# Kernel tuning notes

Measured on AMD Instinct MI355X. Metric: run time of the kernel, lower is better.

## Reference

```python
import jax, jax.numpy as jnp
import numpy as np

NF, IN_NF, N_LAYERS = 64, 196, 3
B, H, W = 1, 256, 256
P3 = [(1, 1), (1, 1)]
P1 = [(0, 0), (0, 0)]


def conv2d(x, w, pad):
    return jax.lax.conv_general_dilated(x, w, (1, 1), pad,
                                        dimension_numbers=('NCHW', 'OIHW', 'NCHW'))


def prelu(x, a):
    return jnp.where(x >= 0, x, a[None, :, None, None] * x)


def warp(x, flow):
    # standard backward bilinear warp, zero padding outside the image
    Bx, C, Hx, Wx = x.shape
    yy, xx = jnp.meshgrid(jnp.arange(Hx, dtype=x.dtype),
                          jnp.arange(Wx, dtype=x.dtype), indexing='ij')
    px = xx[None] + flow[:, 0]  # (B,H,W)
    py = yy[None] + flow[:, 1]

    def sample(img, px, py):  # img (C,H,W); px,py (H,W)
        x0 = jnp.floor(px)
        y0 = jnp.floor(py)
        x1 = x0 + 1.0
        y1 = y0 + 1.0
        wx1 = px - x0
        wx0 = 1.0 - wx1
        wy1 = py - y0
        wy0 = 1.0 - wy1

        def gather(xi, yi):
            valid = (xi >= 0) & (xi <= Wx - 1) & (yi >= 0) & (yi <= Hx - 1)
            xc = jnp.clip(xi, 0, Wx - 1).astype(jnp.int32)
            yc = jnp.clip(yi, 0, Hx - 1).astype(jnp.int32)
            return img[:, yc, xc] * valid.astype(img.dtype)

        return (gather(x0, y0) * (wx0 * wy0) + gather(x1, y0) * (wx1 * wy0)
                + gather(x0, y1) * (wx0 * wy1) + gather(x1, y1) * (wx1 * wy1))

    return jax.vmap(sample)(x, px, py)


def setup_inputs() -> dict:
    key = jax.random.key(0)
    ks = jax.random.split(key, 11)
    s = 0.05
    return {
        'feat_0': jax.random.normal(ks[0], (B, 64, H, W), jnp.float32),
        'feat_1': jax.random.normal(ks[1], (B, 64, H, W), jnp.float32),
        'feat_dense': jax.random.normal(ks[2], (B, 64, H, W), jnp.float32),
        'flow': jax.random.normal(ks[3], (B, 4, H, W), jnp.float32),
        'space_mask': jax.random.uniform(ks[4], (B, 1, H, W), jnp.float32),
        'head_w': jax.random.normal(ks[5], (IN_NF, IN_NF, 3, 3), jnp.float32) * s,
        'head_a': jnp.full((IN_NF,), 0.25, jnp.float32),
        'conv_w': jax.random.normal(ks[6], (N_LAYERS, IN_NF, IN_NF, 3, 3), jnp.float32) * s,
        'conv_a': jnp.full((N_LAYERS, IN_NF), 0.25, jnp.float32),
        'last_w': jax.random.normal(ks[7], (4 + NF, IN_NF * (N_LAYERS + 1), 1, 1), jnp.float32) * s,
        'last_b': jax.random.normal(ks[8], (4 + NF,), jnp.float32) * s,
        'mask_w': jax.random.normal(ks[9], (2, NF, 3, 3), jnp.float32) * s,
        'mask_b': jax.random.normal(ks[10], (2,), jnp.float32) * s,
    }


def reference(feat_0, feat_1, feat_dense, flow, space_mask,
              head_w, head_a, conv_w, conv_a, last_w, last_b, mask_w, mask_b):
    f0 = warp(feat_0, flow[:, :2])
    f1 = warp(feat_1, flow[:, 2:4])
    x = jnp.concatenate([f0, f1, feat_dense, flow], axis=1)  # (B, in_nf, H, W)
    sm_up = jnp.repeat(jnp.repeat(space_mask, 2, axis=2), 2, axis=3)

    # head: conv3x3 -> PReLU, then mask (dense / use_sparsity=False path)
    x = prelu(conv2d(x, head_w, P3), head_a) * space_mask
    outs = [x]
    for i in range(N_LAYERS):
        x = conv2d(x, conv_w[i], P3) * space_mask
        x = prelu(x, conv_a[i])
        outs.append(x)
    x = conv2d(jnp.concatenate(outs, axis=1), last_w, P1) + last_b[None, :, None, None]

    smn = conv2d(x[:, 4:], mask_w, P3) + mask_b[None, :, None, None]

    Bx, Cx, Hx, Wx = x.shape
    x_up = jax.image.resize(x, (Bx, Cx, 2 * Hx, 2 * Wx), method='bilinear')
    smn_up = jax.image.resize(smn, (Bx, 2, 2 * Hx, 2 * Wx), method='bilinear')

    flow_out = x_up[:, :4]
    feat_t = x_up[:, 4:]
    # eval-mode mask (training=False): hard argmax between channel 0 and 1
    mask_next = (smn_up[:, :1] > smn_up[:, 1:2]).astype(x.dtype) * sm_up
    return flow_out, feat_t, mask_next
```

## Files before the change

### kernel.cpp

```cpp
#include <hip/hip_runtime.h>

typedef _Float16 f16;
typedef _Float16 f16x8 __attribute__((ext_vector_type(8)));
typedef _Float16 f16x4 __attribute__((ext_vector_type(4)));
typedef float    f32x4 __attribute__((ext_vector_type(4)));
typedef float    f32x16 __attribute__((ext_vector_type(16)));

#define MFMA16(a,b,c) __builtin_amdgcn_mfma_f32_16x16x32_f16(a,b,c,0,0,0)
#define MFMA32(a,b,c) __builtin_amdgcn_mfma_f32_32x32x16_f16(a,b,c,0,0,0)

#define NPIX 65536
#define PXS   8
#define KHS   2064
#define K16S  4128
#define HS    8256
#define CBS   16512
#define ROWH  115584
#define RBYTES 231168
#define SBUF  ((size_t)258*RBYTES)

#define PKSUB  7168
#define PKCB   43008
#define PK_CONV 903168

#define PKL_CB  5120
#define PKL_BI  35840

#define ASTG 14336
#define BSTG 16640

__global__ void k_pack_conv(const float* __restrict__ head_w,
                            const float* __restrict__ conv_w,
                            f16* __restrict__ dst)
{
    int t = blockIdx.x*256 + threadIdx.x;
    int lane = t & 63; t >>= 6;
    int ob  = t % 7;  t /= 7;
    int sel = t & 1;  t >>= 1;
    int kx  = t % 3;  t /= 3;
    int k16 = t & 1;  t >>= 1;
    int cb  = t % 7;  t /= 7;
    int ky  = t % 3;  t /= 3;
    int li  = t;
    if (li >= 4) return;
    const float* W = (li == 0) ? head_w : (conv_w + (size_t)(li-1)*196*196*9);
    int oc  = ob*32 + (lane & 31);
    int ic0 = cb*32 + k16*16 + (lane >> 5)*8;
    int tap = ky*3 + kx;
    f16x8 v;
#pragma unroll
    for (int j = 0; j < 8; ++j) {
        int ic = ic0 + j;
        float x = 0.f;
        if (oc < 196 && ic < 196) x = W[((size_t)oc*196 + ic)*9 + tap];
        f16 h = (f16)x;
        v[j] = (sel == 0) ? h : (f16)(x - (float)h);
    }
    size_t frag = (((((size_t)(ky*7+cb)*2 + k16)*3 + kx)*2 + sel)*7 + ob);
    *(f16x8*)(dst + (size_t)li*PK_CONV + frag*512 + (size_t)lane*8) = v;
}

__global__ void k_pack_last(const float* __restrict__ last_w, f16* __restrict__ dst)
{
    int t = blockIdx.x*256 + threadIdx.x;
    if (t >= 4*7*5*2*64) return;
    int lane = t & 63; t >>= 6;
    int sel  = t & 1;  t >>= 1;
    int ob   = t % 5;  t /= 5;
    int cb   = t % 7;  t /= 7;
    int bi   = t;
    int oc = ob*16 + (lane & 15);
    int k0 = cb*32 + (lane >> 4)*8;
    f16x8 v;
#pragma unroll
    for (int j = 0; j < 8; ++j) {
        int k = k0 + j;
        float x = 0.f;
        if (oc < 68 && k < 196) x = last_w[(size_t)oc*784 + bi*196 + k];
        f16 h = (f16)x;
        v[j] = (sel == 0) ? h : (f16)(x - (float)h);
    }
    *(f16x8*)(dst + (((size_t)((bi*7+cb)*5 + ob)*2 + sel)*64 + lane)*8) = v;
}

__global__ void k_zero_halo(f16* __restrict__ bufA, f16* __restrict__ bufB)
{
    int c = blockIdx.x*256 + threadIdx.x;
    int end = c & 1; c >>= 1;
    int kh  = c & 1; c >>= 1;
    int k16 = c & 1; c >>= 1;
    int h   = c & 1; c >>= 1;
    int cb  = c % 7; c /= 7;
    int row = c % 258; c /= 258;
    if (c >= 2) return;
    f16* base = (c == 0) ? bufA : bufB;
    f16* p = base + (size_t)row*ROWH + cb*CBS + h*HS + k16*K16S + kh*KHS + (end ? 257 : 0)*PXS;
    f16x8 z = {(f16)0,(f16)0,(f16)0,(f16)0,(f16)0,(f16)0,(f16)0,(f16)0};
    *(f16x8*)p = z;
}

struct Gath { int o00,o01,o10,o11; float w00,w01,w10,w11; };

__device__ inline Gath mk_gath(float pxf, float pyf)
{
    float x0 = floorf(pxf), y0 = floorf(pyf);
    float x1 = x0 + 1.f, y1 = y0 + 1.f;
    float wx1 = pxf - x0, wx0 = 1.f - wx1;
    float wy1 = pyf - y0, wy0 = 1.f - wy1;
    bool vx0 = (x0 >= 0.f) && (x0 <= 255.f);
    bool vx1 = (x1 >= 0.f) && (x1 <= 255.f);
    bool vy0 = (y0 >= 0.f) && (y0 <= 255.f);
    bool vy1 = (y1 >= 0.f) && (y1 <= 255.f);
    int ix0 = min(max((int)x0, 0), 255);
    int ix1 = min(max((int)x1, 0), 255);
    int iy0 = min(max((int)y0, 0), 255);
    int iy1 = min(max((int)y1, 0), 255);
    Gath g;
    g.o00 = iy0*256 + ix0; g.w00 = (vx0 && vy0) ? wx0*wy0 : 0.f;
    g.o01 = iy0*256 + ix1; g.w01 = (vx1 && vy0) ? wx1*wy0 : 0.f;
    g.o10 = iy1*256 + ix0; g.w10 = (vx0 && vy1) ? wx0*wy1 : 0.f;
    g.o11 = iy1*256 + ix1; g.w11 = (vx1 && vy1) ? wx1*wy1 : 0.f;
    return g;
}

__device__ inline void store4n(f16* __restrict__ rowb, int slot, int c0,
                               float a, float b, float c, float d)
{
    f16x4 hi, lo;
    f16 h;
    h = (f16)a; hi[0] = h; lo[0] = (f16)(a - (float)h);
    h = (f16)b; hi[1] = h; lo[1] = (f16)(b - (float)h);
    h = (f16)c; hi[2] = h; lo[2] = (f16)(c - (float)h);
    h = (f16)d; hi[3] = h; lo[3] = (f16)(d - (float)h);
    int cb = c0 >> 5, w32 = c0 & 31;
    f16* p = rowb + cb*CBS + (w32 >> 4)*K16S + ((w32 >> 3) & 1)*KHS
                 + (size_t)slot*PXS + (w32 & 7);
    *(f16x4*)p        = hi;
    *(f16x4*)(p + HS) = lo;
}

__global__ void k_warp_concat(const float* __restrict__ f0, const float* __restrict__ f1,
                              const float* __restrict__ fd, const float* __restrict__ flow,
                              f16* __restrict__ out)
{
    int px = blockIdx.x*256 + threadIdx.x;
    int row = px >> 8, col = px & 255;
    f16* rowb = out + (size_t)(row+1)*ROWH;
    int slot = col + 1;
    Gath g0 = mk_gath((float)col + flow[px],          (float)row + flow[NPIX   + px]);
    Gath g1 = mk_gath((float)col + flow[2*NPIX + px], (float)row + flow[3*NPIX + px]);
#pragma unroll
    for (int c = 0; c < 64; c += 4) {
        float v[4];
#pragma unroll
        for (int r = 0; r < 4; ++r) {
            const float* im = f0 + (size_t)(c+r)*NPIX;
            v[r] = g0.w00*im[g0.o00] + g0.w01*im[g0.o01] + g0.w10*im[g0.o10] + g0.w11*im[g0.o11];
        }
        store4n(rowb, slot, c, v[0], v[1], v[2], v[3]);
    }
#pragma unroll
    for (int c = 0; c < 64; c += 4) {
        float v[4];
#pragma unroll
        for (int r = 0; r < 4; ++r) {
            const float* im = f1 + (size_t)(c+r)*NPIX;
            v[r] = g1.w00*im[g1.o00] + g1.w01*im[g1.o01] + g1.w10*im[g1.o10] + g1.w11*im[g1.o11];
        }
        store4n(rowb, slot, 64 + c, v[0], v[1], v[2], v[3]);
    }
#pragma unroll
    for (int c = 0; c < 64; c += 4) {
        store4n(rowb, slot, 128 + c, fd[(size_t)(c+0)*NPIX + px], fd[(size_t)(c+1)*NPIX + px],
                                     fd[(size_t)(c+2)*NPIX + px], fd[(size_t)(c+3)*NPIX + px]);
    }
    store4n(rowb, slot, 192, flow[px], flow[NPIX+px], flow[2*NPIX+px], flow[3*NPIX+px]);
#pragma unroll
    for (int c = 196; c < 224; c += 4) store4n(rowb, slot, c, 0.f, 0.f, 0.f, 0.f);
}

template<int NOB, int OB0>
__device__ __forceinline__ void micro(const char* __restrict__ ab, const char* __restrict__ bl,
                                      f32x16 (&acc)[4][2], int lane)
{
    f16x8 Bh[2], Bl[2];
    Bh[0] = *(const f16x8*)(bl);
    Bh[1] = *(const f16x8*)(bl + 512);
    Bl[0] = *(const f16x8*)(bl + 8320);
    Bl[1] = *(const f16x8*)(bl + 8320 + 512);
#pragma unroll
    for (int o = 0; o < NOB; ++o) {
        f16x8 Ah = *(const f16x8*)(ab + (OB0 + o)*1024 + lane*16);
        f16x8 Al = *(const f16x8*)(ab + (7 + OB0 + o)*1024 + lane*16);
#pragma unroll
        for (int pt = 0; pt < 2; ++pt) {
            acc[o][pt] = MFMA32(Ah, Bh[pt], acc[o][pt]);
            acc[o][pt] = MFMA32(Al, Bh[pt], acc[o][pt]);
            acc[o][pt] = MFMA32(Ah, Bl[pt], acc[o][pt]);
        }
    }
}

__global__ __launch_bounds__(256, 2)
void k_conv32(const f16* __restrict__ in, f16* __restrict__ out,
              const f16* __restrict__ pack, const float* __restrict__ alpha,
              const float* __restrict__ mask)
{
    __shared__ __align__(16) char As[2][ASTG];
    __shared__ __align__(16) char Bs[2][BSTG];

    int bid = blockIdx.x;
    int wg  = (bid & 7)*64 + (bid >> 3);
    int row  = wg >> 1;
    int half = wg & 1;
    int tid  = threadIdx.x;
    int lane = tid & 63;
    int w    = tid >> 6;
    int ocg  = ((w >> 1) ^ bid) & 1;
    int pxg  = w & 1;
    int l31 = lane & 31, lk = lane >> 5;
    int cb0 = half*128;

    f32x16 acc[4][2];
#pragma unroll
    for (int o = 0; o < 4; ++o)
#pragma unroll
        for (int pt = 0; pt < 2; ++pt)
#pragma unroll
            for (int e = 0; e < 16; ++e) acc[o][pt][e] = 0.f;

    auto stageA = [&](int b, const f16* src) {
        __builtin_amdgcn_global_load_lds(
            (const __attribute__((address_space(1))) void*)(src + (size_t)tid*8),
            (__attribute__((address_space(3))) void*)(&As[b][0] + tid*16), 16, 0, 0);
        __builtin_amdgcn_global_load_lds(
            (const __attribute__((address_space(1))) void*)(src + (size_t)(tid+256)*8),
            (__attribute__((address_space(3))) void*)(&As[b][0] + (tid+256)*16), 16, 0, 0);
        __builtin_amdgcn_global_load_lds(
            (const __attribute__((address_space(1))) void*)(src + (size_t)(tid+512)*8),
            (__attribute__((address_space(3))) void*)(&As[b][0] + (tid+512)*16), 16, 0, 0);
        if (tid < 128)
            __builtin_amdgcn_global_load_lds(
                (const __attribute__((address_space(1))) void*)(src + (size_t)(tid+768)*8),
                (__attribute__((address_space(3))) void*)(&As[b][0] + (tid+768)*16), 16, 0, 0);
    };

    auto stageB = [&](int b, const f16* g) {
#pragma unroll
        for (int u = 0; u < 5; ++u) {
            int c = tid + u*256;
            if (u < 4 || c < 1040) {
                int pl = c / 130;
                int i  = c - pl*130;
                const f16* src = g + (size_t)pl*KHS + (size_t)(cb0 + i)*PXS;
                __builtin_amdgcn_global_load_lds(
                    (const __attribute__((address_space(1))) void*)src,
                    (__attribute__((address_space(3))) void*)(&Bs[b][0] + c*16),
                    16, 0, 0);
            }
        }
    };

    const int lbase = lk*2080 + (pxg*64 + l31)*16;

    const f16* g = in + (size_t)row*ROWH;
    stageB(0, g);
    stageA(0, pack);
    __syncthreads();

    int asel = 0, bsel = 0, cbc = 0, q = 0;
    for (int ph = 0; ph < 21; ++ph) {
        if (ph < 20) {
            if (cbc < 6) { g += CBS; ++cbc; }
            else         { g += ROWH - 6*CBS; cbc = 0; }
            stageB(bsel ^ 1, g);
        }
#pragma unroll
        for (int s = 0; s < 6; ++s) {
            if (q < 125) stageA(asel ^ 1, pack + (size_t)(q+1)*PKSUB);
            const char* ab = &As[asel][0];
            const char* bl = &Bs[bsel][0] + lbase + (s/3)*4160 + (s%3)*16;
            if (ocg == 0) micro<4,0>(ab, bl, acc, lane);
            else          micro<3,4>(ab, bl, acc, lane);
            __syncthreads();
            asel ^= 1; ++q;
        }
        bsel ^= 1;
    }

    int nob = (ocg == 0) ? 4 : 3;
    int ob0 = (ocg == 0) ? 0 : 4;
    int colbase = cb0 + pxg*64;
    float mv[2];
#pragma unroll
    for (int pt = 0; pt < 2; ++pt) mv[pt] = mask[row*256 + colbase + pt*32 + l31];
#pragma unroll
    for (int o = 0; o < 4; ++o) {
        if (o >= nob) continue;
        int ob = ob0 + o;
#pragma unroll
        for (int qg = 0; qg < 4; ++qg) {
            int oc0 = ob*32 + 8*qg + 4*lk;
            f32x4 a4 = *(const f32x4*)(alpha + min(oc0, 192));
#pragma unroll
            for (int pt = 0; pt < 2; ++pt) {
                f16x4 hi, lo;
#pragma unroll
                for (int e = 0; e < 4; ++e) {
                    float v = acc[o][pt][qg*4 + e];
                    v = (v >= 0.f ? v : a4[e]*v) * mv[pt];
                    f16 h = (f16)v;
                    hi[e] = h;
                    lo[e] = (f16)(v - (float)h);
                }
                f16* p = out + (size_t)(row+1)*ROWH + (size_t)(colbase + pt*32 + l31 + 1)*PXS
                       + lk*4 + ob*CBS + (qg >> 1)*K16S + (qg & 1)*KHS;
                *(f16x4*)p        = hi;
                *(f16x4*)(p + HS) = lo;
            }
        }
    }
}

__global__ __launch_bounds__(256, 4)
void k_acc_last(const f16* __restrict__ in, const f16* __restrict__ pack,
                const float* __restrict__ bias, float* __restrict__ accp, int bi)
{
    int lane = threadIdx.x & 63;
    int wid  = (blockIdx.x << 2) | (threadIdx.x >> 6);
    int row  = wid >> 3;
    int col0 = (wid & 7) << 5;
    int l15 = lane & 15, lk = lane >> 4;

    f32x4 acc[5][2];
#pragma unroll
    for (int i = 0; i < 5; ++i)
#pragma unroll
        for (int j = 0; j < 2; ++j)
            acc[i][j] = (f32x4){0.f, 0.f, 0.f, 0.f};

    const f16* bb = in + (size_t)(row+1)*ROWH + (size_t)(col0 + l15 + 1)*PXS
                  + (lk >> 1)*K16S + (lk & 1)*KHS;
    const f16* ap = pack + (size_t)bi*PKL_BI + (size_t)lane*8;
    for (int cb = 0; cb < 7; ++cb) {
        f16x8 bh[2], bl[2];
#pragma unroll
        for (int pb = 0; pb < 2; ++pb) {
            const f16* p = bb + cb*CBS + pb*16*PXS;
            bh[pb] = *(const f16x8*)p;
            bl[pb] = *(const f16x8*)(p + HS);
        }
        const f16* a = ap + cb*PKL_CB;
#pragma unroll
        for (int ob = 0; ob < 5; ++ob) {
            f16x8 ah = *(const f16x8*)(a + ob*1024);
            f16x8 al = *(const f16x8*)(a + ob*1024 + 512);
#pragma unroll
            for (int pb = 0; pb < 2; ++pb) {
                acc[ob][pb] = MFMA16(ah, bh[pb], acc[ob][pb]);
                acc[ob][pb] = MFMA16(ah, bl[pb], acc[ob][pb]);
                acc[ob][pb] = MFMA16(al, bh[pb], acc[ob][pb]);
            }
        }
    }
#pragma unroll
    for (int ob = 0; ob < 5; ++ob) {
        int oc0 = ob*16 + lk*4;
        if (oc0 >= 72) continue;
#pragma unroll
        for (int pb = 0; pb < 2; ++pb) {
            int px = row*256 + col0 + pb*16 + l15;
            float* dst = accp + (size_t)px*72 + oc0;
            f32x4 d = acc[ob][pb];
            if (bi == 0) {
                f32x4 b4;
#pragma unroll
                for (int r = 0; r < 4; ++r) b4[r] = bias[min(oc0 + r, 67)];
                *(f32x4*)dst = d + b4;
            } else {
                *(f32x4*)dst = *(const f32x4*)dst + d;
            }
        }
    }
}

__global__ void k_smn(const float* __restrict__ accp, const float* __restrict__ mw,
                      const float* __restrict__ mb, float* __restrict__ smn)
{
    int px = blockIdx.x*256 + threadIdx.x;
    int row = px >> 8, col = px & 255;
    float s0 = mb[0], s1 = mb[1];
    for (int ky = 0; ky < 3; ++ky) {
        int r = row + ky - 1;
        if ((unsigned)r > 255u) continue;
        for (int kx = 0; kx < 3; ++kx) {
            int c = col + kx - 1;
            if ((unsigned)c > 255u) continue;
            const float* ab = accp + ((size_t)r*256 + c)*72 + 4;
            const float* w  = mw + ky*3 + kx;
#pragma unroll
            for (int ch = 0; ch < 64; ch += 4) {
                f32x4 v = *(const f32x4*)(ab + ch);
                s0 += v[0]*w[(ch+0)*9] + v[1]*w[(ch+1)*9] + v[2]*w[(ch+2)*9] + v[3]*w[(ch+3)*9];
                s1 += v[0]*w[(64+ch+0)*9] + v[1]*w[(64+ch+1)*9] + v[2]*w[(64+ch+2)*9] + v[3]*w[(64+ch+3)*9];
            }
        }
    }
    smn[px]        = s0;
    smn[NPIX + px] = s1;
}

__global__ void k_upsample(const float* __restrict__ accp, float* __restrict__ outp)
{
    int o = blockIdx.x*256 + threadIdx.x;
    int oy = o >> 9, ox = o & 511;
    int my = oy >> 1, mx = ox >> 1;
    int r0, r1, c0, c1; float wy0, wy1, wx0, wx1;
    if (oy & 1) { r0 = my;            r1 = min(my+1, 255); wy0 = 0.75f; wy1 = 0.25f; }
    else        { r0 = max(my-1, 0);  r1 = my;             wy0 = 0.25f; wy1 = 0.75f; }
    if (ox & 1) { c0 = mx;            c1 = min(mx+1, 255); wx0 = 0.75f; wx1 = 0.25f; }
    else        { c0 = max(mx-1, 0);  c1 = mx;             wx0 = 0.25f; wx1 = 0.75f; }
    const float* p00 = accp + ((size_t)r0*256 + c0)*72;
    const float* p01 = accp + ((size_t)r0*256 + c1)*72;
    const float* p10 = accp + ((size_t)r1*256 + c0)*72;
    const float* p11 = accp + ((size_t)r1*256 + c1)*72;
    float w00 = wy0*wx0, w01 = wy0*wx1, w10 = wy1*wx0, w11 = wy1*wx1;
#pragma unroll
    for (int ch = 0; ch < 68; ch += 4) {
        f32x4 va = *(const f32x4*)(p00 + ch);
        f32x4 vb = *(const f32x4*)(p01 + ch);
        f32x4 vc = *(const f32x4*)(p10 + ch);
        f32x4 vd = *(const f32x4*)(p11 + ch);
        f32x4 v;
#pragma unroll
        for (int r = 0; r < 4; ++r)
            v[r] = w00*va[r] + w01*vb[r] + w10*vc[r] + w11*vd[r];
        outp[(size_t)(ch+0)*262144 + o] = v[0];
        outp[(size_t)(ch+1)*262144 + o] = v[1];
        outp[(size_t)(ch+2)*262144 + o] = v[2];
        outp[(size_t)(ch+3)*262144 + o] = v[3];
    }
}

__global__ void k_mask(const float* __restrict__ smn, const float* __restrict__ sm,
                       float* __restrict__ outp)
{
    int o = blockIdx.x*256 + threadIdx.x;
    int oy = o >> 9, ox = o & 511;
    int my = oy >> 1, mx = ox >> 1;
    int r0, r1, c0, c1; float wy0, wy1, wx0, wx1;
    if (oy & 1) { r0 = my;            r1 = min(my+1, 255); wy0 = 0.75f; wy1 = 0.25f; }
    else        { r0 = max(my-1, 0);  r1 = my;             wy0 = 0.25f; wy1 = 0.75f; }
    if (ox & 1) { c0 = mx;            c1 = min(mx+1, 255); wx0 = 0.75f; wx1 = 0.25f; }
    else        { c0 = max(mx-1, 0);  c1 = mx;             wx0 = 0.25f; wx1 = 0.75f; }
    float w00 = wy0*wx0, w01 = wy0*wx1, w10 = wy1*wx0, w11 = wy1*wx1;
    int i00 = r0*256 + c0, i01 = r0*256 + c1, i10 = r1*256 + c0, i11 = r1*256 + c1;
    float s0 = w00*smn[i00] + w01*smn[i01] + w10*smn[i10] + w11*smn[i11];
    float s1 = w00*smn[NPIX+i00] + w01*smn[NPIX+i01] + w10*smn[NPIX+i10] + w11*smn[NPIX+i11];
    outp[(size_t)68*262144 + o] = (s0 > s1) ? sm[my*256 + mx] : 0.f;
}

extern "C" void kernel_launch(void* const* d_in, const int* in_sizes, int n_in,
                              void* d_out, int out_size, void* d_ws, size_t ws_size,
                              hipStream_t stream)
{
    const float* feat0  = (const float*)d_in[0];
    const float* feat1  = (const float*)d_in[1];
    const float* featd  = (const float*)d_in[2];
    const float* flow   = (const float*)d_in[3];
    const float* smask  = (const float*)d_in[4];
    const float* head_w = (const float*)d_in[5];
    const float* head_a = (const float*)d_in[6];
    const float* conv_w = (const float*)d_in[7];
    const float* conv_a = (const float*)d_in[8];
    const float* last_w = (const float*)d_in[9];
    const float* last_b = (const float*)d_in[10];
    const float* mask_w = (const float*)d_in[11];
    const float* mask_b = (const float*)d_in[12];
    float* outp = (float*)d_out;

    char* ws = (char*)d_ws;
    size_t off = 0;
    f16* bufA = (f16*)(ws + off); off += SBUF;
    f16* bufB = (f16*)(ws + off); off += SBUF;
    f16* packc = (f16*)(ws + off); off += (size_t)4*PK_CONV*2;
    f16* packl = (f16*)(ws + off); off += (size_t)4*PKL_BI*2;
    float* accp = (float*)(ws + off); off += (size_t)NPIX*72*4;
    float* smn  = (float*)(ws + off); off += (size_t)2*NPIX*4;

    hipMemsetAsync(bufA, 0, RBYTES, stream);
    hipMemsetAsync((char*)bufA + (size_t)257*RBYTES, 0, RBYTES, stream);
    hipMemsetAsync(bufB, 0, RBYTES, stream);
    hipMemsetAsync((char*)bufB + (size_t)257*RBYTES, 0, RBYTES, stream);
    k_zero_halo<<<226, 256, 0, stream>>>(bufA, bufB);

    k_pack_conv<<<1764, 256, 0, stream>>>(head_w, conv_w, packc);
    k_pack_last<<<70, 256, 0, stream>>>(last_w, packl);
    k_warp_concat<<<256, 256, 0, stream>>>(feat0, feat1, featd, flow, bufA);

    k_conv32<<<512, 256, 0, stream>>>(bufA, bufB, packc, head_a, smask);
    k_acc_last<<<512, 256, 0, stream>>>(bufB, packl, last_b, accp, 0);
    k_conv32<<<512, 256, 0, stream>>>(bufB, bufA, packc + (size_t)1*PK_CONV, conv_a, smask);
    k_acc_last<<<512, 256, 0, stream>>>(bufA, packl, last_b, accp, 1);
    k_conv32<<<512, 256, 0, stream>>>(bufA, bufB, packc + (size_t)2*PK_CONV, conv_a + 196, smask);
    k_acc_last<<<512, 256, 0, stream>>>(bufB, packl, last_b, accp, 2);
    k_conv32<<<512, 256, 0, stream>>>(bufB, bufA, packc + (size_t)3*PK_CONV, conv_a + 392, smask);
    k_acc_last<<<512, 256, 0, stream>>>(bufA, packl, last_b, accp, 3);

    k_smn<<<256, 256, 0, stream>>>(accp, mask_w, mask_b, smn);
    k_upsample<<<1024, 256, 0, stream>>>(accp, outp);
    k_mask<<<1024, 256, 0, stream>>>(smn, smask, outp);
}
```

Baseline: 806.5 us.

## Triple-buffer weight staging with explicit vmcnt waits in conv kernel

The weight (A) tiles in the conv kernel move from double to triple buffering, prefetched two steps ahead. Each __syncthreads is replaced by a partial s_waitcnt vmcnt plus s_barrier, so outstanding global-to-LDS loads can stay in flight across iterations. stageB now issues a uniform load count per thread (a clamped fifth load into padding), and MFMA sections run under raised s_setprio. This adds LDS use, which could cut occupancy, and relies on hand-counted vmcnt values being correct.

Result: slower. 861.5 us (+6.8%).

```diff
diff --git a/kernel.cpp b/kernel.cpp
--- a/kernel.cpp
+++ b/kernel.cpp
@@ -27,7 +27,7 @@
 #define PKL_BI  35840
 
 #define ASTG 14336
-#define BSTG 16640
+#define BSTG 17408
 
 __global__ void k_pack_conv(const float* __restrict__ head_w,
                             const float* __restrict__ conv_w,
@@ -206,7 +206,7 @@
               const f16* __restrict__ pack, const float* __restrict__ alpha,
               const float* __restrict__ mask)
 {
-    __shared__ __align__(16) char As[2][ASTG];
+    __shared__ __align__(16) char As[3][ASTG];
     __shared__ __align__(16) char Bs[2][BSTG];
 
     int bid = blockIdx.x;
@@ -230,35 +230,37 @@
             for (int e = 0; e < 16; ++e) acc[o][pt][e] = 0.f;
 
     auto stageA = [&](int b, const f16* src) {
+#pragma unroll
+        for (int u = 0; u < 3; ++u) {
+            int c = tid + u*256;
+            __builtin_amdgcn_global_load_lds(
+                (const __attribute__((address_space(1))) void*)(src + (size_t)c*8),
+                (__attribute__((address_space(3))) void*)(&As[b][0] + c*16), 16, 0, 0);
+        }
+        int c4 = 768 + (tid & 127);
         __builtin_amdgcn_global_load_lds(
-            (const __attribute__((address_space(1))) void*)(src + (size_t)tid*8),
-            (__attribute__((address_space(3))) void*)(&As[b][0] + tid*16), 16, 0, 0);
+            (const __attribute__((address_space(1))) void*)(src + (size_t)c4*8),
+            (__attribute__((address_space(3))) void*)(&As[b][0] + c4*16), 16, 0, 0);
+    };
+
+    auto stageB = [&](int b, const f16* g) {
+#pragma unroll
+        for (int u = 0; u < 4; ++u) {
+            int c = tid + u*256;
+            int pl = c / 130;
+            int i  = c - pl*130;
+            const f16* src = g + (size_t)pl*KHS + (size_t)(cb0 + i)*PXS;
+            __builtin_amdgcn_global_load_lds(
+                (const __attribute__((address_space(1))) void*)src,
+                (__attribute__((address_space(3))) void*)(&Bs[b][0] + c*16),
+                16, 0, 0);
+        }
+        int c5 = min(1024 + lane, 1039);
+        const f16* src5 = g + (size_t)7*KHS + (size_t)(cb0 + (c5 - 910))*PXS;
         __builtin_amdgcn_global_load_lds(
-            (const __attribute__((address_space(1))) void*)(src + (size_t)(tid+256)*8),
-            (__attribute__((address_space(3))) void*)(&As[b][0] + (tid+256)*16), 16, 0, 0);
-        __builtin_amdgcn_global_load_lds(
-            (const __attribute__((address_space(1))) void*)(src + (size_t)(tid+512)*8),
-            (__attribute__((address_space(3))) void*)(&As[b][0] + (tid+512)*16), 16, 0, 0);
-        if (tid < 128)
-            __builtin_amdgcn_global_load_lds(
-                (const __attribute__((address_space(1))) void*)(src + (size_t)(tid+768)*8),
-                (__attribute__((address_space(3))) void*)(&As[b][0] + (tid+768)*16), 16, 0, 0);
-    };
-
-    auto stageB = [&](int b, const f16* g) {
-#pragma unroll
-        for (int u = 0; u < 5; ++u) {
-            int c = tid + u*256;
-            if (u < 4 || c < 1040) {
-                int pl = c / 130;
-                int i  = c - pl*130;
-                const f16* src = g + (size_t)pl*KHS + (size_t)(cb0 + i)*PXS;
-                __builtin_amdgcn_global_load_lds(
-                    (const __attribute__((address_space(1))) void*)src,
-                    (__attribute__((address_space(3))) void*)(&Bs[b][0] + c*16),
-                    16, 0, 0);
-            }
-        }
+            (const __attribute__((address_space(1))) void*)src5,
+            (__attribute__((address_space(3))) void*)(&Bs[b][0] + 16384),
+            16, 0, 0);
     };
 
     const int lbase = lk*2080 + (pxg*64 + l31)*16;
@@ -266,24 +268,40 @@
     const f16* g = in + (size_t)row*ROWH;
     stageB(0, g);
     stageA(0, pack);
-    __syncthreads();
-
-    int asel = 0, bsel = 0, cbc = 0, q = 0;
+    stageA(1, pack + PKSUB);
+    asm volatile("s_waitcnt vmcnt(4)" ::: "memory");
+    __builtin_amdgcn_s_barrier();
+
+    int bsel = 0, cbc = 0, q = 0;
     for (int ph = 0; ph < 21; ++ph) {
-        if (ph < 20) {
-            if (cbc < 6) { g += CBS; ++cbc; }
-            else         { g += ROWH - 6*CBS; cbc = 0; }
-            stageB(bsel ^ 1, g);
-        }
 #pragma unroll
         for (int s = 0; s < 6; ++s) {
-            if (q < 125) stageA(asel ^ 1, pack + (size_t)(q+1)*PKSUB);
-            const char* ab = &As[asel][0];
+            bool bphase = (s == 0) && (ph < 20);
+            if (bphase) {
+                if (cbc < 6) { g += CBS; ++cbc; }
+                else         { g += ROWH - 6*CBS; cbc = 0; }
+                stageB(bsel ^ 1, g);
+            }
+            if (q < 124) {
+                int nb = q + 2;
+                int bsl = nb - (nb/3)*3;
+                stageA(bsl, pack + (size_t)nb*PKSUB);
+            }
+            const char* ab = &As[q - (q/3)*3][0];
             const char* bl = &Bs[bsel][0] + lbase + (s/3)*4160 + (s%3)*16;
+            __builtin_amdgcn_s_setprio(1);
             if (ocg == 0) micro<4,0>(ab, bl, acc, lane);
             else          micro<3,4>(ab, bl, acc, lane);
-            __syncthreads();
-            asel ^= 1; ++q;
+            __builtin_amdgcn_s_setprio(0);
+            if (q < 124) {
+                if (bphase) asm volatile("s_waitcnt vmcnt(9)" ::: "memory");
+                else        asm volatile("s_waitcnt vmcnt(4)" ::: "memory");
+                __builtin_amdgcn_s_barrier();
+            } else if (q == 124) {
+                asm volatile("s_waitcnt vmcnt(0)" ::: "memory");
+                __builtin_amdgcn_s_barrier();
+            }
+            ++q;
         }
         bsel ^= 1;
     }
```

## Skip zero-padded K16 sub-block, triple-buffer weight stages, raise MFMA priority

Applied to the files above, without the earlier changes.

The weight packing now leaves out the final half input-channel block (channels 208-223, which are all zero padding for 196 channels) and compacts the layout to 117 micro-steps per layer instead of 126. The conv loop is restructured into explicit ky/cb/k16/kx loops that skip that half block, cutting wasted MFMA work and weight loads. Weight staging in LDS moves from double to triple buffering with a prefetch distance of two, and MFMA sections are wrapped in s_setprio. The extra LDS buffer may lower occupancy, and the loop is no longer fully unrolled.

Result: no change. 804.2 us (-0.3%).

```diff
diff --git a/kernel.cpp b/kernel.cpp
--- a/kernel.cpp
+++ b/kernel.cpp
@@ -20,8 +20,8 @@
 #define SBUF  ((size_t)258*RBYTES)
 
 #define PKSUB  7168
-#define PKCB   43008
 #define PK_CONV 903168
+#define NMICRO 117
 
 #define PKL_CB  5120
 #define PKL_BI  35840
@@ -43,6 +43,7 @@
     int ky  = t % 3;  t /= 3;
     int li  = t;
     if (li >= 4) return;
+    if (cb == 6 && k16 == 1) return;
     const float* W = (li == 0) ? head_w : (conv_w + (size_t)(li-1)*196*196*9);
     int oc  = ob*32 + (lane & 31);
     int ic0 = cb*32 + k16*16 + (lane >> 5)*8;
@@ -56,8 +57,9 @@
         f16 h = (f16)x;
         v[j] = (sel == 0) ? h : (f16)(x - (float)h);
     }
-    size_t frag = (((((size_t)(ky*7+cb)*2 + k16)*3 + kx)*2 + sel)*7 + ob);
-    *(f16x8*)(dst + (size_t)li*PK_CONV + frag*512 + (size_t)lane*8) = v;
+    int pos = ky*39 + ((cb < 6) ? (cb*6 + k16*3 + kx) : (36 + kx));
+    *(f16x8*)(dst + (size_t)li*PK_CONV + (size_t)pos*PKSUB
+              + (size_t)(sel*7 + ob)*512 + (size_t)lane*8) = v;
 }
 
 __global__ void k_pack_last(const float* __restrict__ last_w, f16* __restrict__ dst)
@@ -206,7 +208,7 @@
               const f16* __restrict__ pack, const float* __restrict__ alpha,
               const float* __restrict__ mask)
 {
-    __shared__ __align__(16) char As[2][ASTG];
+    __shared__ __align__(16) char As[3][ASTG];
     __shared__ __align__(16) char Bs[2][BSTG];
 
     int bid = blockIdx.x;
@@ -266,26 +268,39 @@
     const f16* g = in + (size_t)row*ROWH;
     stageB(0, g);
     stageA(0, pack);
+    stageA(1, pack + PKSUB);
     __syncthreads();
 
-    int asel = 0, bsel = 0, cbc = 0, q = 0;
-    for (int ph = 0; ph < 21; ++ph) {
-        if (ph < 20) {
-            if (cbc < 6) { g += CBS; ++cbc; }
-            else         { g += ROWH - 6*CBS; cbc = 0; }
-            stageB(bsel ^ 1, g);
-        }
-#pragma unroll
-        for (int s = 0; s < 6; ++s) {
-            if (q < 125) stageA(asel ^ 1, pack + (size_t)(q+1)*PKSUB);
-            const char* ab = &As[asel][0];
-            const char* bl = &Bs[bsel][0] + lbase + (s/3)*4160 + (s%3)*16;
-            if (ocg == 0) micro<4,0>(ab, bl, acc, lane);
-            else          micro<3,4>(ab, bl, acc, lane);
-            __syncthreads();
-            asel ^= 1; ++q;
-        }
-        bsel ^= 1;
+    int bsel = 0;
+    int q = 0;
+    for (int ky = 0; ky < 3; ++ky) {
+        for (int cb = 0; cb < 7; ++cb) {
+            int nk16 = (cb == 6) ? 1 : 2;
+            bool lastPhase = (ky == 2) && (cb == 6);
+            if (!lastPhase) {
+                const f16* gn = (cb < 6) ? (g + CBS) : (g + ROWH - 6*CBS);
+                stageB(bsel ^ 1, gn);
+                g = gn;
+            }
+            for (int k16 = 0; k16 < nk16; ++k16) {
+#pragma unroll
+                for (int kx = 0; kx < 3; ++kx) {
+                    if (q + 2 < NMICRO) {
+                        int nb = q + 2;
+                        stageA(nb - (nb/3)*3, pack + (size_t)nb*PKSUB);
+                    }
+                    const char* ab = &As[q - (q/3)*3][0];
+                    const char* bl = &Bs[bsel][0] + lbase + k16*4160 + kx*16;
+                    __builtin_amdgcn_s_setprio(1);
+                    if (ocg == 0) micro<4,0>(ab, bl, acc, lane);
+                    else          micro<3,4>(ab, bl, acc, lane);
+                    __builtin_amdgcn_s_setprio(0);
+                    __syncthreads();
+                    ++q;
+                }
+            }
+            bsel ^= 1;
+        }
     }
 
     int nob = (ocg == 0) ? 4 : 3;
```
